# Kernel optimization log

Hardware: AMD Instinct MI355X
Metric: run time of the kernel (lower is better)

## Reference

```python
import jax, jax.numpy as jnp
import numpy as np

N_NODES = 100000
N_EDGES = 1600000
D = 128


def setup_inputs() -> dict:
    key = jax.random.key(0)
    k1, k2, k3, k4 = jax.random.split(key, 4)
    x = jax.random.normal(k1, (N_NODES, D), dtype=jnp.float32)
    # scale weights by 1/sqrt(fan_in) (matches typical init, keeps exp(e) stable)
    W = jax.random.normal(k2, (D, D), dtype=jnp.float32) / np.sqrt(D)
    a = jax.random.normal(k3, (2 * D,), dtype=jnp.float32) / np.sqrt(2 * D)
    edge_index = jax.random.randint(k4, (2, N_EDGES), 0, N_NODES, dtype=jnp.int64)
    return {"x": x, "W": W, "a": a, "edge_index": edge_index}


def reference(x, W, a, edge_index):
    # x: [N, in], W: [out, in] (torch Linear layout), a: [2*out], edge_index: [2, E]
    N = x.shape[0]
    d_out = W.shape[0]
    h = x @ W.T                                   # [N, out]
    src = edge_index[0]
    tgt = edge_index[1]
    # a(cat([h_src, h_tgt])) == h_src @ a[:d] + h_tgt @ a[d:] — avoids [E, 2d] concat
    s_src = h @ a[:d_out]                         # [N]
    s_tgt = h @ a[d_out:]                         # [N]
    e = jax.nn.leaky_relu(s_src[src] + s_tgt[tgt], negative_slope=0.2)  # [E]
    att = jnp.exp(e)                              # [E]
    att_sum = jax.ops.segment_sum(att, tgt, num_segments=N)             # [N]
    att_norm = att / (att_sum[tgt] + 1e-8)        # [E] (dropout=0 / eval mode)
    h_prime = jax.ops.segment_sum(h[src] * att_norm[:, None], tgt, num_segments=N)  # [N, out]
    h_prime = h_prime + x                          # residual (in_features == out_features)
    return jax.nn.elu(h_prime)
```

## Files before the change

kernel.cpp:

```cpp
#include <hip/hip_runtime.h>
#include <hip/hip_bf16.h>

#define DD 128
#define CAP 56
#define NBPW 128
#define CHUNK 4096
#define LBIN 832

typedef _Float16 half8  __attribute__((ext_vector_type(8)));
typedef _Float16 half2t __attribute__((ext_vector_type(2)));
typedef float f32x4 __attribute__((ext_vector_type(4)));

__device__ __forceinline__ ushort h16bits(float f) {
    _Float16 h = (_Float16)f;
    return __builtin_bit_cast(ushort, h);
}
__device__ __forceinline__ half8 pack8h(float4 lo, float4 hi) {
    half8 r;
    r[0] = (_Float16)lo.x; r[1] = (_Float16)lo.y;
    r[2] = (_Float16)lo.z; r[3] = (_Float16)lo.w;
    r[4] = (_Float16)hi.x; r[5] = (_Float16)hi.y;
    r[6] = (_Float16)hi.z; r[7] = (_Float16)hi.w;
    return r;
}
__device__ __forceinline__ float fdot2u(uint pair, uint avp, float c) {
    return __builtin_amdgcn_fdot2(__builtin_bit_cast(half2t, pair),
                                  __builtin_bit_cast(half2t, avp), c, false);
}

__global__ __launch_bounds__(256) void prep_w(
    const float* __restrict__ W, _Float16* __restrict__ Wh) {
    int i = blockIdx.x * 256 + threadIdx.x;
    if (i < DD * DD) Wh[i] = (_Float16)W[i];
}

__global__ __launch_bounds__(256, 2) void gemm_hist_kernel(
    const float* __restrict__ x, const _Float16* __restrict__ Wh,
    const float* __restrict__ a, ushort* __restrict__ h,
    float* __restrict__ ssrc, float* __restrict__ stgt,
    const int* __restrict__ tgt, int* __restrict__ H,
    int N, int E, int nbin, int nblk) {
    __shared__ ushort hl[4][16][136];
    __shared__ int lh[LBIN];
    const int wid = threadIdx.x >> 6;
    const int l   = threadIdx.x & 63;
    const int lr  = l & 15;
    const int lk  = l >> 4;

    half8 Bf[4][8];
    #pragma unroll
    for (int kt = 0; kt < 4; ++kt)
        #pragma unroll
        for (int n = 0; n < 8; ++n)
            Bf[kt][n] = *(const half8*)(Wh + (size_t)(n * 16 + lr) * DD + kt * 32 + lk * 8);
    float avs[8], avt[8];
    #pragma unroll
    for (int n = 0; n < 8; ++n) {
        avs[n] = a[n * 16 + lr];
        avt[n] = a[DD + n * 16 + lr];
    }

    const int rowBase = blockIdx.x * 64 + wid * 16;
    const int arow = rowBase + lr;
    f32x4 acc[8];
    #pragma unroll
    for (int n = 0; n < 8; ++n) acc[n] = (f32x4){0.f, 0.f, 0.f, 0.f};

    #pragma unroll
    for (int kt = 0; kt < 4; ++kt) {
        float4 x0, x1;
        if (arow < N) {
            const float* xp = x + (size_t)arow * DD + kt * 32 + lk * 8;
            x0 = *(const float4*)xp;
            x1 = *(const float4*)(xp + 4);
        } else {
            x0 = make_float4(0.f, 0.f, 0.f, 0.f);
            x1 = x0;
        }
        half8 A = pack8h(x0, x1);
        #pragma unroll
        for (int n = 0; n < 8; ++n)
            acc[n] = __builtin_amdgcn_mfma_f32_16x16x32_f16(A, Bf[kt][n], acc[n], 0, 0, 0);
    }

    float ps[4] = {0.f, 0.f, 0.f, 0.f}, pt[4] = {0.f, 0.f, 0.f, 0.f};
    #pragma unroll
    for (int n = 0; n < 8; ++n)
        #pragma unroll
        for (int r = 0; r < 4; ++r) {
            ps[r] = fmaf(acc[n][r], avs[n], ps[r]);
            pt[r] = fmaf(acc[n][r], avt[n], pt[r]);
        }
    #pragma unroll
    for (int r = 0; r < 4; ++r) {
        #pragma unroll
        for (int m = 8; m >= 1; m >>= 1) {
            ps[r] += __shfl_xor(ps[r], m);
            pt[r] += __shfl_xor(pt[r], m);
        }
    }
    if (lr == 0) {
        #pragma unroll
        for (int r = 0; r < 4; ++r) {
            int grow = rowBase + lk * 4 + r;
            if (grow < N) { ssrc[grow] = ps[r]; stgt[grow] = pt[r]; }
        }
    }

    #pragma unroll
    for (int n = 0; n < 8; ++n)
        #pragma unroll
        for (int r = 0; r < 4; ++r)
            hl[wid][lk * 4 + r][n * 16 + lr] = h16bits(acc[n][r]);
    __syncthreads();
    if (arow < N) {
        uint4* dst = (uint4*)(h + (size_t)arow * DD + lk * 32);
        const uint4* s4 = (const uint4*)&hl[wid][lr][lk * 32];
        dst[0] = s4[0]; dst[1] = s4[1]; dst[2] = s4[2]; dst[3] = s4[3];
    }

    if (blockIdx.x < nblk) {
        const int blk = blockIdx.x;
        for (int i = threadIdx.x; i < nbin; i += 256) lh[i] = 0;
        __syncthreads();
        const int base = blk * CHUNK;
        const int end = min(E, base + CHUNK);
        for (int e = base + threadIdx.x; e < end; e += 256)
            atomicAdd(&lh[tgt[e] >> 7], 1);
        __syncthreads();
        for (int i = threadIdx.x; i < nbin; i += 256) H[i * nblk + blk] = lh[i];
    }
}

__global__ __launch_bounds__(256) void p2a_colscan(
    int* __restrict__ H, int* __restrict__ binTot, int nblk) {
    __shared__ int lds[256];
    const int o = blockIdx.x * nblk;
    const int t = threadIdx.x;
    int a0 = (2 * t     < nblk) ? H[o + 2 * t]     : 0;
    int a1 = (2 * t + 1 < nblk) ? H[o + 2 * t + 1] : 0;
    int s = a0 + a1;
    lds[t] = s;
    __syncthreads();
    int val = s;
    for (int off = 1; off < 256; off <<= 1) {
        int u = (t >= off) ? lds[t - off] : 0;
        __syncthreads();
        val += u;
        lds[t] = val;
        __syncthreads();
    }
    int excl = val - s;
    if (2 * t     < nblk) H[o + 2 * t]     = excl;
    if (2 * t + 1 < nblk) H[o + 2 * t + 1] = excl + a0;
    if (t == 255) binTot[blockIdx.x] = val;
}

__device__ __forceinline__ void scan_bins(const int* __restrict__ binTot,
                                          int* __restrict__ binOffL, int nbin) {
    __shared__ int lds[256];
    const int t = threadIdx.x;
    int v[4];
    int s = 0;
    #pragma unroll
    for (int j = 0; j < 4; ++j) {
        int idx = t * 4 + j;
        v[j] = (idx < nbin) ? binTot[idx] : 0;
        s += v[j];
    }
    lds[t] = s;
    __syncthreads();
    int val = s;
    for (int off = 1; off < 256; off <<= 1) {
        int u = (t >= off) ? lds[t - off] : 0;
        __syncthreads();
        val += u;
        lds[t] = val;
        __syncthreads();
    }
    int excl = val - s;
    #pragma unroll
    for (int j = 0; j < 4; ++j) {
        int idx = t * 4 + j;
        if (idx < nbin) binOffL[idx] = excl;
        excl += v[j];
    }
    __syncthreads();
}

__global__ __launch_bounds__(256) void p3_partition(
    const int* __restrict__ src, const int* __restrict__ tgt,
    const int* __restrict__ H, const int* __restrict__ binTot,
    uint* __restrict__ ebuf, int E, int nbin, int nblk) {
    __shared__ int binOffL[LBIN];
    __shared__ int lcur[LBIN];
    scan_bins(binTot, binOffL, nbin);
    const int blk = blockIdx.x;
    for (int i = threadIdx.x; i < nbin; i += 256) lcur[i] = 0;
    __syncthreads();
    const int base = blk * CHUNK;
    const int end = min(E, base + CHUNK);
    for (int e = base + threadIdx.x; e < end; e += 256) {
        int s = src[e], t = tgt[e];
        int tb = t >> 7;
        int r = atomicAdd(&lcur[tb], 1);
        int slot = binOffL[tb] + H[tb * nblk + blk] + r;
        ebuf[slot] = ((uint)(t & 127) << 17) | (uint)s;
    }
}

__global__ __launch_bounds__(256) void p4_bucket(
    const uint* __restrict__ ebuf, const int* __restrict__ binTot,
    int* __restrict__ srcS, int* __restrict__ deg, int N, int nbin) {
    __shared__ int binOffL[LBIN];
    __shared__ int cur[NBPW];
    scan_bins(binTot, binOffL, nbin);
    const int bin = blockIdx.x;
    const int n0 = bin * NBPW;
    for (int i = threadIdx.x; i < NBPW; i += 256) cur[i] = 0;
    __syncthreads();
    const int beg = binOffL[bin];
    const int end = beg + binTot[bin];
    for (int i = beg + threadIdx.x; i < end; i += 256) {
        uint v = ebuf[i];
        int tl = (int)(v >> 17);
        int s  = (int)(v & 0x1FFFFu);
        int pos = atomicAdd(&cur[tl], 1);
        if (pos < CAP) srcS[(size_t)(n0 + tl) * CAP + pos] = s;
    }
    __syncthreads();
    for (int i = threadIdx.x; i < NBPW; i += 256) {
        int node = n0 + i;
        if (node < N) deg[node] = cur[i];
    }
}

__global__ __launch_bounds__(256) void gather_acc_kernel(
    const int* __restrict__ srcS, const int* __restrict__ degA,
    const float* __restrict__ ssrc, const float* __restrict__ stgt,
    const ushort* __restrict__ h, const float* __restrict__ x,
    float* __restrict__ out, int N) {
    __shared__ uint lds_pv[8][64];
    const int tid  = threadIdx.x;
    const int wid  = tid >> 6, lane = tid & 63;
    const int hw   = lane >> 5, hl = lane & 31;
    const int g    = hl >> 4,   l4 = hl & 15;
    const int nib  = (wid << 1) | hw;
    const int node = blockIdx.x * 8 + nib;
    if (node >= N) return;

    const float4 xv = *(const float4*)(x + (size_t)node * DD + l4 * 8 + g * 4);
    int deg = degA[node];
    if (deg > CAP) deg = CAP;
    const float st = stgt[node];
    const size_t base = (size_t)node * CAP;

    int sv0 = 0, sv1 = 0;
    float att0 = 0.f, att1 = 0.f;
    if (hl < deg) {
        sv0 = srcS[base + hl];
        float v = ssrc[sv0] + st;
        v = v > 0.f ? v : 0.2f * v;
        att0 = __expf(v);
    }
    if (hl + 32 < deg) {
        sv1 = srcS[base + hl + 32];
        float v = ssrc[sv1] + st;
        v = v > 0.f ? v : 0.2f * v;
        att1 = __expf(v);
    }
    float asum = att0 + att1;
    #pragma unroll
    for (int m = 16; m >= 1; m >>= 1) asum += __shfl_xor(asum, m);
    const float inv = 1.f / (asum + 1e-8f);
    lds_pv[nib][hl]      = ((uint)h16bits(att0) << 17) | (uint)sv0;
    lds_pv[nib][hl + 32] = ((uint)h16bits(att1) << 17) | (uint)sv1;

    const int passes = (deg + 1) >> 1;
    const uint* pvrow = lds_pv[nib];
    float acc[8] = {0.f, 0.f, 0.f, 0.f, 0.f, 0.f, 0.f, 0.f};

    #define PAIR_STEP(pv0, pv1)                                                  \
    {                                                                            \
        int s0 = (int)((pv0) & 0x1FFFFu), s1 = (int)((pv1) & 0x1FFFFu);          \
        uint4 hv0 = *(const uint4*)(h + ((size_t)s0 << 7) + (l4 << 3));          \
        uint4 hv1 = *(const uint4*)(h + ((size_t)s1 << 7) + (l4 << 3));          \
        uint avp = ((pv0) >> 17) | (((pv1) >> 17) << 16);                        \
        uint p0, p1;                                                             \
        p0 = __builtin_amdgcn_perm(hv1.x, hv0.x, 0x05040100u);                   \
        p1 = __builtin_amdgcn_perm(hv1.x, hv0.x, 0x07060302u);                   \
        acc[0] = fdot2u(p0, avp, acc[0]); acc[1] = fdot2u(p1, avp, acc[1]);      \
        p0 = __builtin_amdgcn_perm(hv1.y, hv0.y, 0x05040100u);                   \
        p1 = __builtin_amdgcn_perm(hv1.y, hv0.y, 0x07060302u);                   \
        acc[2] = fdot2u(p0, avp, acc[2]); acc[3] = fdot2u(p1, avp, acc[3]);      \
        p0 = __builtin_amdgcn_perm(hv1.z, hv0.z, 0x05040100u);                   \
        p1 = __builtin_amdgcn_perm(hv1.z, hv0.z, 0x07060302u);                   \
        acc[4] = fdot2u(p0, avp, acc[4]); acc[5] = fdot2u(p1, avp, acc[5]);      \
        p0 = __builtin_amdgcn_perm(hv1.w, hv0.w, 0x05040100u);                   \
        p1 = __builtin_amdgcn_perm(hv1.w, hv0.w, 0x07060302u);                   \
        acc[6] = fdot2u(p0, avp, acc[6]); acc[7] = fdot2u(p1, avp, acc[7]);      \
    }

    int p = 0;
    for (; p + 4 <= passes; p += 4) {
        const int i0 = (p << 1) + g;
        uint a0 = pvrow[i0], a1 = pvrow[i0 + 2];
        uint a2 = pvrow[i0 + 4], a3 = pvrow[i0 + 6];
        PAIR_STEP(a0, a1);
        PAIR_STEP(a2, a3);
    }
    if (p + 2 <= passes) {
        const int i0 = (p << 1) + g;
        uint a0 = pvrow[i0], a1 = pvrow[i0 + 2];
        PAIR_STEP(a0, a1);
        p += 2;
    }
    if (p < passes) {
        const int i0 = (p << 1) + g;
        uint a0 = pvrow[i0];
        int s0 = (int)(a0 & 0x1FFFFu);
        uint avp = a0 >> 17;
        uint4 hv0 = *(const uint4*)(h + ((size_t)s0 << 7) + (l4 << 3));
        acc[0] = fdot2u(hv0.x, avp, acc[0]); acc[1] = fdot2u(hv0.x >> 16, avp, acc[1]);
        acc[2] = fdot2u(hv0.y, avp, acc[2]); acc[3] = fdot2u(hv0.y >> 16, avp, acc[3]);
        acc[4] = fdot2u(hv0.z, avp, acc[4]); acc[5] = fdot2u(hv0.z >> 16, avp, acc[5]);
        acc[6] = fdot2u(hv0.w, avp, acc[6]); acc[7] = fdot2u(hv0.w >> 16, avp, acc[7]);
    }
    #undef PAIR_STEP

    #pragma unroll
    for (int j = 0; j < 8; ++j) acc[j] += __shfl_xor(acc[j], 16);

    float a0 = g ? acc[4] : acc[0];
    float a1 = g ? acc[5] : acc[1];
    float a2 = g ? acc[6] : acc[2];
    float a3 = g ? acc[7] : acc[3];
    float o0 = fmaf(a0, inv, xv.x), o1 = fmaf(a1, inv, xv.y);
    float o2 = fmaf(a2, inv, xv.z), o3 = fmaf(a3, inv, xv.w);
    o0 = o0 > 0.f ? o0 : expm1f(o0);
    o1 = o1 > 0.f ? o1 : expm1f(o1);
    o2 = o2 > 0.f ? o2 : expm1f(o2);
    o3 = o3 > 0.f ? o3 : expm1f(o3);
    *(float4*)(out + (size_t)node * DD + l4 * 8 + g * 4) = make_float4(o0, o1, o2, o3);
}

extern "C" void kernel_launch(void* const* d_in, const int* in_sizes, int n_in,
                              void* d_out, int out_size, void* d_ws, size_t ws_size,
                              hipStream_t stream) {
    const float* x  = (const float*)d_in[0];
    const float* W  = (const float*)d_in[1];
    const float* a  = (const float*)d_in[2];
    const int*   ei = (const int*)d_in[3];

    const int N = in_sizes[0] / DD;
    const int E = in_sizes[3] / 2;
    const int* src = ei;
    const int* tgt = ei + E;

    float* out = (float*)d_out;

    const int nbin = (N + NBPW - 1) / NBPW;
    const int nblk = (E + CHUNK - 1) / CHUNK;
    const int nTiles = (N + 63) / 64;

    char* w = (char*)d_ws;
    int*      srcS   = (int*)w;               w += (size_t)N * CAP * 4;
    ushort*   h      = (ushort*)w;            w += (size_t)N * DD * 2;
    float*    ssrc   = (float*)w;             w += (size_t)N * 4;
    float*    stgt   = (float*)w;             w += (size_t)N * 4;
    int*      deg    = (int*)w;               w += (size_t)N * 4;
    uint*     ebuf   = (uint*)w;              w += (size_t)E * 4;
    _Float16* Wh     = (_Float16*)w;          w += (size_t)DD * DD * 2;
    int*      H      = (int*)w;               w += (size_t)nbin * nblk * 4;
    int*      binTot = (int*)w;               w += (size_t)nbin * 4;

    prep_w<<<(DD * DD + 255) / 256, 256, 0, stream>>>(W, Wh);
    gemm_hist_kernel<<<nTiles, 256, 0, stream>>>(x, Wh, a, h, ssrc, stgt,
                                                 tgt, H, N, E, nbin, nblk);
    p2a_colscan<<<nbin, 256, 0, stream>>>(H, binTot, nblk);
    p3_partition<<<nblk, 256, 0, stream>>>(src, tgt, H, binTot, ebuf, E, nbin, nblk);
    p4_bucket<<<nbin, 256, 0, stream>>>(ebuf, binTot, srcS, deg, N, nbin);
    gather_acc_kernel<<<(N + 7) / 8, 256, 0, stream>>>(srcS, deg, ssrc, stgt,
                                                       h, x, out, N);
}
```

Baseline: 162.7 us.

## Shrink edge chunks, store histogram as ushort, cache per-block offsets in LDS

Cuts the edge chunk size from 4096 to 1024. This gives about four times more partition blocks, and spreads the histogram work across every GEMM block instead of only the first few hundred. To offset the larger block-by-bin histogram, the counts are stored as 16-bit values, and the column scan now processes eight entries per thread. The partition kernel loads its column of histogram offsets into shared memory once, instead of reading global memory on every edge. The risks are 16-bit overflow if a bin ever holds more than 65535 edges, and extra per-block overhead from the scan_bins prologue that each of the additional partition blocks repeats.

Result: slower. 174.7 us (+7.4%).

```diff
diff --git a/kernel.cpp b/kernel.cpp
--- a/kernel.cpp
+++ b/kernel.cpp
@@ -4,7 +4,7 @@
 #define DD 128
 #define CAP 56
 #define NBPW 128
-#define CHUNK 4096
+#define CHUNK 1024
 #define LBIN 832
 
 typedef _Float16 half8  __attribute__((ext_vector_type(8)));
@@ -38,7 +38,7 @@
     const float* __restrict__ x, const _Float16* __restrict__ Wh,
     const float* __restrict__ a, ushort* __restrict__ h,
     float* __restrict__ ssrc, float* __restrict__ stgt,
-    const int* __restrict__ tgt, int* __restrict__ H,
+    const int* __restrict__ tgt, ushort* __restrict__ H,
     int N, int E, int nbin, int nblk) {
     __shared__ ushort hl[4][16][136];
     __shared__ int lh[LBIN];
@@ -128,18 +128,24 @@
         for (int e = base + threadIdx.x; e < end; e += 256)
             atomicAdd(&lh[tgt[e] >> 7], 1);
         __syncthreads();
-        for (int i = threadIdx.x; i < nbin; i += 256) H[i * nblk + blk] = lh[i];
+        for (int i = threadIdx.x; i < nbin; i += 256)
+            H[(size_t)i * nblk + blk] = (ushort)lh[i];
     }
 }
 
 __global__ __launch_bounds__(256) void p2a_colscan(
-    int* __restrict__ H, int* __restrict__ binTot, int nblk) {
+    ushort* __restrict__ H, int* __restrict__ binTot, int nblk) {
     __shared__ int lds[256];
-    const int o = blockIdx.x * nblk;
+    const size_t o = (size_t)blockIdx.x * nblk;
     const int t = threadIdx.x;
-    int a0 = (2 * t     < nblk) ? H[o + 2 * t]     : 0;
-    int a1 = (2 * t + 1 < nblk) ? H[o + 2 * t + 1] : 0;
-    int s = a0 + a1;
+    int v[8];
+    int s = 0;
+    #pragma unroll
+    for (int j = 0; j < 8; ++j) {
+        int idx = t * 8 + j;
+        v[j] = (idx < nblk) ? (int)H[o + idx] : 0;
+        s += v[j];
+    }
     lds[t] = s;
     __syncthreads();
     int val = s;
@@ -151,8 +157,12 @@
         __syncthreads();
     }
     int excl = val - s;
-    if (2 * t     < nblk) H[o + 2 * t]     = excl;
-    if (2 * t + 1 < nblk) H[o + 2 * t + 1] = excl + a0;
+    #pragma unroll
+    for (int j = 0; j < 8; ++j) {
+        int idx = t * 8 + j;
+        if (idx < nblk) H[o + idx] = (ushort)excl;
+        excl += v[j];
+    }
     if (t == 255) binTot[blockIdx.x] = val;
 }
 
@@ -190,13 +200,17 @@
 
 __global__ __launch_bounds__(256) void p3_partition(
     const int* __restrict__ src, const int* __restrict__ tgt,
-    const int* __restrict__ H, const int* __restrict__ binTot,
+    const ushort* __restrict__ H, const int* __restrict__ binTot,
     uint* __restrict__ ebuf, int E, int nbin, int nblk) {
     __shared__ int binOffL[LBIN];
     __shared__ int lcur[LBIN];
+    __shared__ int HcolL[LBIN];
     scan_bins(binTot, binOffL, nbin);
     const int blk = blockIdx.x;
-    for (int i = threadIdx.x; i < nbin; i += 256) lcur[i] = 0;
+    for (int i = threadIdx.x; i < nbin; i += 256) {
+        lcur[i] = 0;
+        HcolL[i] = (int)H[(size_t)i * nblk + blk];
+    }
     __syncthreads();
     const int base = blk * CHUNK;
     const int end = min(E, base + CHUNK);
@@ -204,7 +218,7 @@
         int s = src[e], t = tgt[e];
         int tb = t >> 7;
         int r = atomicAdd(&lcur[tb], 1);
-        int slot = binOffL[tb] + H[tb * nblk + blk] + r;
+        int slot = binOffL[tb] + HcolL[tb] + r;
         ebuf[slot] = ((uint)(t & 127) << 17) | (uint)s;
     }
 }
@@ -371,7 +385,7 @@
     int*      deg    = (int*)w;               w += (size_t)N * 4;
     uint*     ebuf   = (uint*)w;              w += (size_t)E * 4;
     _Float16* Wh     = (_Float16*)w;          w += (size_t)DD * DD * 2;
-    int*      H      = (int*)w;               w += (size_t)nbin * nblk * 4;
+    ushort*   H      = (ushort*)w;            w += (size_t)nbin * nblk * 2;
     int*      binTot = (int*)w;               w += (size_t)nbin * 4;
 
     prep_w<<<(DD * DD + 255) / 256, 256, 0, stream>>>(W, Wh);
```

## Fuse bucketing into gather via LDS buckets, shrink bins, compact histogram

Applied to the files above, without the earlier changes.

The per-bin bucket pass and the per-node gather kernel are merged into one kernel. It builds each 64-node bin's source lists in shared memory and then computes attention and aggregation for those nodes directly. This removes the global srcS/deg round trip and one launch. The histogram is stored as ushort in a blk-major layout, and the bin prefix scan moves into a single dedicated kernel instead of being redone in every block. The fused kernel launches far fewer blocks, each processing 8 nodes per wave serially, which risks lower parallelism and latency hiding in the gather.

Measured after the change: 160.6 us. About the same (-1.3%).

```diff
diff --git a/kernel.cpp b/kernel.cpp
--- a/kernel.cpp
+++ b/kernel.cpp
@@ -3,9 +3,9 @@
 
 #define DD 128
 #define CAP 56
-#define NBPW 128
+#define NBPW 64
 #define CHUNK 4096
-#define LBIN 832
+#define LBIN 1600
 
 typedef _Float16 half8  __attribute__((ext_vector_type(8)));
 typedef _Float16 half2t __attribute__((ext_vector_type(2)));
@@ -38,7 +38,7 @@
     const float* __restrict__ x, const _Float16* __restrict__ Wh,
     const float* __restrict__ a, ushort* __restrict__ h,
     float* __restrict__ ssrc, float* __restrict__ stgt,
-    const int* __restrict__ tgt, int* __restrict__ H,
+    const int* __restrict__ tgt, ushort* __restrict__ H,
     int N, int E, int nbin, int nblk) {
     __shared__ ushort hl[4][16][136];
     __shared__ int lh[LBIN];
@@ -126,19 +126,20 @@
         const int base = blk * CHUNK;
         const int end = min(E, base + CHUNK);
         for (int e = base + threadIdx.x; e < end; e += 256)
-            atomicAdd(&lh[tgt[e] >> 7], 1);
-        __syncthreads();
-        for (int i = threadIdx.x; i < nbin; i += 256) H[i * nblk + blk] = lh[i];
+            atomicAdd(&lh[tgt[e] >> 6], 1);
+        __syncthreads();
+        ushort* Hrow = H + (size_t)blk * nbin;
+        for (int i = threadIdx.x; i < nbin; i += 256) Hrow[i] = (ushort)lh[i];
     }
 }
 
 __global__ __launch_bounds__(256) void p2a_colscan(
-    int* __restrict__ H, int* __restrict__ binTot, int nblk) {
+    ushort* __restrict__ H, int* __restrict__ binTot, int nbin, int nblk) {
     __shared__ int lds[256];
-    const int o = blockIdx.x * nblk;
+    const int bin = blockIdx.x;
     const int t = threadIdx.x;
-    int a0 = (2 * t     < nblk) ? H[o + 2 * t]     : 0;
-    int a1 = (2 * t + 1 < nblk) ? H[o + 2 * t + 1] : 0;
+    int a0 = (2 * t     < nblk) ? (int)H[(size_t)(2 * t)     * nbin + bin] : 0;
+    int a1 = (2 * t + 1 < nblk) ? (int)H[(size_t)(2 * t + 1) * nbin + bin] : 0;
     int s = a0 + a1;
     lds[t] = s;
     __syncthreads();
@@ -151,20 +152,20 @@
         __syncthreads();
     }
     int excl = val - s;
-    if (2 * t     < nblk) H[o + 2 * t]     = excl;
-    if (2 * t + 1 < nblk) H[o + 2 * t + 1] = excl + a0;
+    if (2 * t     < nblk) H[(size_t)(2 * t)     * nbin + bin] = (ushort)excl;
+    if (2 * t + 1 < nblk) H[(size_t)(2 * t + 1) * nbin + bin] = (ushort)(excl + a0);
     if (t == 255) binTot[blockIdx.x] = val;
 }
 
-__device__ __forceinline__ void scan_bins(const int* __restrict__ binTot,
-                                          int* __restrict__ binOffL, int nbin) {
+__global__ __launch_bounds__(256) void p2b_binscan(
+    const int* __restrict__ binTot, int* __restrict__ binOff, int nbin) {
     __shared__ int lds[256];
     const int t = threadIdx.x;
-    int v[4];
+    int v[8];
     int s = 0;
     #pragma unroll
-    for (int j = 0; j < 4; ++j) {
-        int idx = t * 4 + j;
+    for (int j = 0; j < 8; ++j) {
+        int idx = t * 8 + j;
         v[j] = (idx < nbin) ? binTot[idx] : 0;
         s += v[j];
     }
@@ -180,168 +181,164 @@
     }
     int excl = val - s;
     #pragma unroll
-    for (int j = 0; j < 4; ++j) {
-        int idx = t * 4 + j;
-        if (idx < nbin) binOffL[idx] = excl;
+    for (int j = 0; j < 8; ++j) {
+        int idx = t * 8 + j;
+        if (idx < nbin) binOff[idx] = excl;
         excl += v[j];
     }
-    __syncthreads();
+    if (t == 255) binOff[nbin] = val;
 }
 
 __global__ __launch_bounds__(256) void p3_partition(
     const int* __restrict__ src, const int* __restrict__ tgt,
-    const int* __restrict__ H, const int* __restrict__ binTot,
+    const ushort* __restrict__ H, const int* __restrict__ binOff,
     uint* __restrict__ ebuf, int E, int nbin, int nblk) {
-    __shared__ int binOffL[LBIN];
+    __shared__ int slotBase[LBIN];
     __shared__ int lcur[LBIN];
-    scan_bins(binTot, binOffL, nbin);
     const int blk = blockIdx.x;
-    for (int i = threadIdx.x; i < nbin; i += 256) lcur[i] = 0;
+    const ushort* Hrow = H + (size_t)blk * nbin;
+    for (int i = threadIdx.x; i < nbin; i += 256) {
+        slotBase[i] = binOff[i] + (int)Hrow[i];
+        lcur[i] = 0;
+    }
     __syncthreads();
     const int base = blk * CHUNK;
     const int end = min(E, base + CHUNK);
     for (int e = base + threadIdx.x; e < end; e += 256) {
         int s = src[e], t = tgt[e];
-        int tb = t >> 7;
+        int tb = t >> 6;
         int r = atomicAdd(&lcur[tb], 1);
-        int slot = binOffL[tb] + H[tb * nblk + blk] + r;
-        ebuf[slot] = ((uint)(t & 127) << 17) | (uint)s;
-    }
-}
-
-__global__ __launch_bounds__(256) void p4_bucket(
-    const uint* __restrict__ ebuf, const int* __restrict__ binTot,
-    int* __restrict__ srcS, int* __restrict__ deg, int N, int nbin) {
-    __shared__ int binOffL[LBIN];
-    __shared__ int cur[NBPW];
-    scan_bins(binTot, binOffL, nbin);
-    const int bin = blockIdx.x;
-    const int n0 = bin * NBPW;
-    for (int i = threadIdx.x; i < NBPW; i += 256) cur[i] = 0;
-    __syncthreads();
-    const int beg = binOffL[bin];
-    const int end = beg + binTot[bin];
-    for (int i = beg + threadIdx.x; i < end; i += 256) {
-        uint v = ebuf[i];
-        int tl = (int)(v >> 17);
-        int s  = (int)(v & 0x1FFFFu);
-        int pos = atomicAdd(&cur[tl], 1);
-        if (pos < CAP) srcS[(size_t)(n0 + tl) * CAP + pos] = s;
-    }
-    __syncthreads();
-    for (int i = threadIdx.x; i < NBPW; i += 256) {
-        int node = n0 + i;
-        if (node < N) deg[node] = cur[i];
-    }
-}
-
-__global__ __launch_bounds__(256) void gather_acc_kernel(
-    const int* __restrict__ srcS, const int* __restrict__ degA,
+        int slot = slotBase[tb] + r;
+        ebuf[slot] = ((uint)(t & 63) << 17) | (uint)s;
+    }
+}
+
+__global__ __launch_bounds__(256) void bucket_gather_kernel(
+    const uint* __restrict__ ebuf, const int* __restrict__ binOff,
     const float* __restrict__ ssrc, const float* __restrict__ stgt,
     const ushort* __restrict__ h, const float* __restrict__ x,
     float* __restrict__ out, int N) {
+    __shared__ uint bucket[NBPW][CAP];
+    __shared__ int  cur[NBPW];
     __shared__ uint lds_pv[8][64];
-    const int tid  = threadIdx.x;
-    const int wid  = tid >> 6, lane = tid & 63;
-    const int hw   = lane >> 5, hl = lane & 31;
-    const int g    = hl >> 4,   l4 = hl & 15;
-    const int nib  = (wid << 1) | hw;
-    const int node = blockIdx.x * 8 + nib;
-    if (node >= N) return;
-
-    const float4 xv = *(const float4*)(x + (size_t)node * DD + l4 * 8 + g * 4);
-    int deg = degA[node];
-    if (deg > CAP) deg = CAP;
-    const float st = stgt[node];
-    const size_t base = (size_t)node * CAP;
-
-    int sv0 = 0, sv1 = 0;
-    float att0 = 0.f, att1 = 0.f;
-    if (hl < deg) {
-        sv0 = srcS[base + hl];
-        float v = ssrc[sv0] + st;
-        v = v > 0.f ? v : 0.2f * v;
-        att0 = __expf(v);
-    }
-    if (hl + 32 < deg) {
-        sv1 = srcS[base + hl + 32];
-        float v = ssrc[sv1] + st;
-        v = v > 0.f ? v : 0.2f * v;
-        att1 = __expf(v);
-    }
-    float asum = att0 + att1;
-    #pragma unroll
-    for (int m = 16; m >= 1; m >>= 1) asum += __shfl_xor(asum, m);
-    const float inv = 1.f / (asum + 1e-8f);
-    lds_pv[nib][hl]      = ((uint)h16bits(att0) << 17) | (uint)sv0;
-    lds_pv[nib][hl + 32] = ((uint)h16bits(att1) << 17) | (uint)sv1;
-
-    const int passes = (deg + 1) >> 1;
-    const uint* pvrow = lds_pv[nib];
-    float acc[8] = {0.f, 0.f, 0.f, 0.f, 0.f, 0.f, 0.f, 0.f};
-
-    #define PAIR_STEP(pv0, pv1)                                                  \
-    {                                                                            \
-        int s0 = (int)((pv0) & 0x1FFFFu), s1 = (int)((pv1) & 0x1FFFFu);          \
-        uint4 hv0 = *(const uint4*)(h + ((size_t)s0 << 7) + (l4 << 3));          \
-        uint4 hv1 = *(const uint4*)(h + ((size_t)s1 << 7) + (l4 << 3));          \
-        uint avp = ((pv0) >> 17) | (((pv1) >> 17) << 16);                        \
-        uint p0, p1;                                                             \
-        p0 = __builtin_amdgcn_perm(hv1.x, hv0.x, 0x05040100u);                   \
-        p1 = __builtin_amdgcn_perm(hv1.x, hv0.x, 0x07060302u);                   \
-        acc[0] = fdot2u(p0, avp, acc[0]); acc[1] = fdot2u(p1, avp, acc[1]);      \
-        p0 = __builtin_amdgcn_perm(hv1.y, hv0.y, 0x05040100u);                   \
-        p1 = __builtin_amdgcn_perm(hv1.y, hv0.y, 0x07060302u);                   \
-        acc[2] = fdot2u(p0, avp, acc[2]); acc[3] = fdot2u(p1, avp, acc[3]);      \
-        p0 = __builtin_amdgcn_perm(hv1.z, hv0.z, 0x05040100u);                   \
-        p1 = __builtin_amdgcn_perm(hv1.z, hv0.z, 0x07060302u);                   \
-        acc[4] = fdot2u(p0, avp, acc[4]); acc[5] = fdot2u(p1, avp, acc[5]);      \
-        p0 = __builtin_amdgcn_perm(hv1.w, hv0.w, 0x05040100u);                   \
-        p1 = __builtin_amdgcn_perm(hv1.w, hv0.w, 0x07060302u);                   \
-        acc[6] = fdot2u(p0, avp, acc[6]); acc[7] = fdot2u(p1, avp, acc[7]);      \
-    }
-
-    int p = 0;
-    for (; p + 4 <= passes; p += 4) {
-        const int i0 = (p << 1) + g;
-        uint a0 = pvrow[i0], a1 = pvrow[i0 + 2];
-        uint a2 = pvrow[i0 + 4], a3 = pvrow[i0 + 6];
-        PAIR_STEP(a0, a1);
-        PAIR_STEP(a2, a3);
-    }
-    if (p + 2 <= passes) {
-        const int i0 = (p << 1) + g;
-        uint a0 = pvrow[i0], a1 = pvrow[i0 + 2];
-        PAIR_STEP(a0, a1);
-        p += 2;
-    }
-    if (p < passes) {
-        const int i0 = (p << 1) + g;
-        uint a0 = pvrow[i0];
-        int s0 = (int)(a0 & 0x1FFFFu);
-        uint avp = a0 >> 17;
-        uint4 hv0 = *(const uint4*)(h + ((size_t)s0 << 7) + (l4 << 3));
-        acc[0] = fdot2u(hv0.x, avp, acc[0]); acc[1] = fdot2u(hv0.x >> 16, avp, acc[1]);
-        acc[2] = fdot2u(hv0.y, avp, acc[2]); acc[3] = fdot2u(hv0.y >> 16, avp, acc[3]);
-        acc[4] = fdot2u(hv0.z, avp, acc[4]); acc[5] = fdot2u(hv0.z >> 16, avp, acc[5]);
-        acc[6] = fdot2u(hv0.w, avp, acc[6]); acc[7] = fdot2u(hv0.w >> 16, avp, acc[7]);
-    }
-    #undef PAIR_STEP
-
-    #pragma unroll
-    for (int j = 0; j < 8; ++j) acc[j] += __shfl_xor(acc[j], 16);
-
-    float a0 = g ? acc[4] : acc[0];
-    float a1 = g ? acc[5] : acc[1];
-    float a2 = g ? acc[6] : acc[2];
-    float a3 = g ? acc[7] : acc[3];
-    float o0 = fmaf(a0, inv, xv.x), o1 = fmaf(a1, inv, xv.y);
-    float o2 = fmaf(a2, inv, xv.z), o3 = fmaf(a3, inv, xv.w);
-    o0 = o0 > 0.f ? o0 : expm1f(o0);
-    o1 = o1 > 0.f ? o1 : expm1f(o1);
-    o2 = o2 > 0.f ? o2 : expm1f(o2);
-    o3 = o3 > 0.f ? o3 : expm1f(o3);
-    *(float4*)(out + (size_t)node * DD + l4 * 8 + g * 4) = make_float4(o0, o1, o2, o3);
+    const int bin = blockIdx.x;
+    const int n0 = bin << 6;
+    const int tid = threadIdx.x;
+
+    for (int i = tid; i < NBPW; i += 256) cur[i] = 0;
+    __syncthreads();
+    const int beg = binOff[bin], end = binOff[bin + 1];
+    for (int i = beg + tid; i < end; i += 256) {
+        uint v = ebuf[i];
+        int tl = (int)(v >> 17);
+        int pos = atomicAdd(&cur[tl], 1);
+        if (pos < CAP) bucket[tl][pos] = v & 0x1FFFFu;
+    }
+    __syncthreads();
+
+    const int wid = tid >> 6, lane = tid & 63;
+    const int hw = lane >> 5, hl = lane & 31;
+    const int g  = hl >> 4,   l4 = hl & 15;
+    const int nib = (wid << 1) | hw;
+
+    for (int it = 0; it < 8; ++it) {
+        const int nloc = (wid << 4) + (it << 1) + hw;
+        const int node = n0 + nloc;
+        if (node >= N) continue;
+
+        const float4 xv = *(const float4*)(x + (size_t)node * DD + l4 * 8 + g * 4);
+        int deg = cur[nloc];
+        if (deg > CAP) deg = CAP;
+        const float st = stgt[node];
+
+        int sv0 = 0, sv1 = 0;
+        float att0 = 0.f, att1 = 0.f;
+        if (hl < deg) {
+            sv0 = (int)bucket[nloc][hl];
+            float v = ssrc[sv0] + st;
+            v = v > 0.f ? v : 0.2f * v;
+            att0 = __expf(v);
+        }
+        if (hl + 32 < deg) {
+            sv1 = (int)bucket[nloc][hl + 32];
+            float v = ssrc[sv1] + st;
+            v = v > 0.f ? v : 0.2f * v;
+            att1 = __expf(v);
+        }
+        float asum = att0 + att1;
+        #pragma unroll
+        for (int m = 16; m >= 1; m >>= 1) asum += __shfl_xor(asum, m);
+        const float inv = 1.f / (asum + 1e-8f);
+        lds_pv[nib][hl]      = ((uint)h16bits(att0) << 17) | (uint)sv0;
+        lds_pv[nib][hl + 32] = ((uint)h16bits(att1) << 17) | (uint)sv1;
+
+        const int passes = (deg + 1) >> 1;
+        const uint* pvrow = lds_pv[nib];
+        float acc[8] = {0.f, 0.f, 0.f, 0.f, 0.f, 0.f, 0.f, 0.f};
+
+        #define PAIR_STEP(pv0, pv1)                                              \
+        {                                                                        \
+            int s0 = (int)((pv0) & 0x1FFFFu), s1 = (int)((pv1) & 0x1FFFFu);      \
+            uint4 hv0 = *(const uint4*)(h + ((size_t)s0 << 7) + (l4 << 3));      \
+            uint4 hv1 = *(const uint4*)(h + ((size_t)s1 << 7) + (l4 << 3));      \
+            uint avp = ((pv0) >> 17) | (((pv1) >> 17) << 16);                    \
+            uint p0, p1;                                                         \
+            p0 = __builtin_amdgcn_perm(hv1.x, hv0.x, 0x05040100u);               \
+            p1 = __builtin_amdgcn_perm(hv1.x, hv0.x, 0x07060302u);               \
+            acc[0] = fdot2u(p0, avp, acc[0]); acc[1] = fdot2u(p1, avp, acc[1]);  \
+            p0 = __builtin_amdgcn_perm(hv1.y, hv0.y, 0x05040100u);               \
+            p1 = __builtin_amdgcn_perm(hv1.y, hv0.y, 0x07060302u);               \
+            acc[2] = fdot2u(p0, avp, acc[2]); acc[3] = fdot2u(p1, avp, acc[3]);  \
+            p0 = __builtin_amdgcn_perm(hv1.z, hv0.z, 0x05040100u);               \
+            p1 = __builtin_amdgcn_perm(hv1.z, hv0.z, 0x07060302u);               \
+            acc[4] = fdot2u(p0, avp, acc[4]); acc[5] = fdot2u(p1, avp, acc[5]);  \
+            p0 = __builtin_amdgcn_perm(hv1.w, hv0.w, 0x05040100u);               \
+            p1 = __builtin_amdgcn_perm(hv1.w, hv0.w, 0x07060302u);               \
+            acc[6] = fdot2u(p0, avp, acc[6]); acc[7] = fdot2u(p1, avp, acc[7]);  \
+        }
+
+        int p = 0;
+        for (; p + 4 <= passes; p += 4) {
+            const int i0 = (p << 1) + g;
+            uint a0 = pvrow[i0], a1 = pvrow[i0 + 2];
+            uint a2 = pvrow[i0 + 4], a3 = pvrow[i0 + 6];
+            PAIR_STEP(a0, a1);
+            PAIR_STEP(a2, a3);
+        }
+        if (p + 2 <= passes) {
+            const int i0 = (p << 1) + g;
+            uint a0 = pvrow[i0], a1 = pvrow[i0 + 2];
+            PAIR_STEP(a0, a1);
+            p += 2;
+        }
+        if (p < passes) {
+            const int i0 = (p << 1) + g;
+            uint a0 = pvrow[i0];
+            int s0 = (int)(a0 & 0x1FFFFu);
+            uint avp = a0 >> 17;
+            uint4 hv0 = *(const uint4*)(h + ((size_t)s0 << 7) + (l4 << 3));
+            acc[0] = fdot2u(hv0.x, avp, acc[0]); acc[1] = fdot2u(hv0.x >> 16, avp, acc[1]);
+            acc[2] = fdot2u(hv0.y, avp, acc[2]); acc[3] = fdot2u(hv0.y >> 16, avp, acc[3]);
+            acc[4] = fdot2u(hv0.z, avp, acc[4]); acc[5] = fdot2u(hv0.z >> 16, avp, acc[5]);
+            acc[6] = fdot2u(hv0.w, avp, acc[6]); acc[7] = fdot2u(hv0.w >> 16, avp, acc[7]);
+        }
+        #undef PAIR_STEP
+
+        #pragma unroll
+        for (int j = 0; j < 8; ++j) acc[j] += __shfl_xor(acc[j], 16);
+
+        float a0 = g ? acc[4] : acc[0];
+        float a1 = g ? acc[5] : acc[1];
+        float a2 = g ? acc[6] : acc[2];
+        float a3 = g ? acc[7] : acc[3];
+        float o0 = fmaf(a0, inv, xv.x), o1 = fmaf(a1, inv, xv.y);
+        float o2 = fmaf(a2, inv, xv.z), o3 = fmaf(a3, inv, xv.w);
+        o0 = o0 > 0.f ? o0 : expm1f(o0);
+        o1 = o1 > 0.f ? o1 : expm1f(o1);
+        o2 = o2 > 0.f ? o2 : expm1f(o2);
+        o3 = o3 > 0.f ? o3 : expm1f(o3);
+        *(float4*)(out + (size_t)node * DD + l4 * 8 + g * 4) = make_float4(o0, o1, o2, o3);
+    }
 }
 
 extern "C" void kernel_launch(void* const* d_in, const int* in_sizes, int n_in,
@@ -363,23 +360,24 @@
     const int nblk = (E + CHUNK - 1) / CHUNK;
     const int nTiles = (N + 63) / 64;
 
+    #define ALIGN256(v) (((size_t)(v) + 255) & ~(size_t)255)
     char* w = (char*)d_ws;
-    int*      srcS   = (int*)w;               w += (size_t)N * CAP * 4;
-    ushort*   h      = (ushort*)w;            w += (size_t)N * DD * 2;
-    float*    ssrc   = (float*)w;             w += (size_t)N * 4;
-    float*    stgt   = (float*)w;             w += (size_t)N * 4;
-    int*      deg    = (int*)w;               w += (size_t)N * 4;
-    uint*     ebuf   = (uint*)w;              w += (size_t)E * 4;
-    _Float16* Wh     = (_Float16*)w;          w += (size_t)DD * DD * 2;
-    int*      H      = (int*)w;               w += (size_t)nbin * nblk * 4;
-    int*      binTot = (int*)w;               w += (size_t)nbin * 4;
+    ushort*   h      = (ushort*)w;            w += ALIGN256((size_t)N * DD * 2);
+    float*    ssrc   = (float*)w;             w += ALIGN256((size_t)N * 4);
+    float*    stgt   = (float*)w;             w += ALIGN256((size_t)N * 4);
+    uint*     ebuf   = (uint*)w;              w += ALIGN256((size_t)E * 4);
+    _Float16* Wh     = (_Float16*)w;          w += ALIGN256((size_t)DD * DD * 2);
+    ushort*   H      = (ushort*)w;            w += ALIGN256((size_t)nblk * nbin * 2);
+    int*      binTot = (int*)w;               w += ALIGN256((size_t)nbin * 4);
+    int*      binOff = (int*)w;               w += ALIGN256((size_t)(nbin + 1) * 4);
+    #undef ALIGN256
 
     prep_w<<<(DD * DD + 255) / 256, 256, 0, stream>>>(W, Wh);
     gemm_hist_kernel<<<nTiles, 256, 0, stream>>>(x, Wh, a, h, ssrc, stgt,
                                                  tgt, H, N, E, nbin, nblk);
-    p2a_colscan<<<nbin, 256, 0, stream>>>(H, binTot, nblk);
-    p3_partition<<<nblk, 256, 0, stream>>>(src, tgt, H, binTot, ebuf, E, nbin, nblk);
-    p4_bucket<<<nbin, 256, 0, stream>>>(ebuf, binTot, srcS, deg, N, nbin);
-    gather_acc_kernel<<<(N + 7) / 8, 256, 0, stream>>>(srcS, deg, ssrc, stgt,
-                                                       h, x, out, N);
-}
+    p2a_colscan<<<nbin, 256, 0, stream>>>(H, binTot, nbin, nblk);
+    p2b_binscan<<<1, 256, 0, stream>>>(binTot, binOff, nbin);
+    p3_partition<<<nblk, 256, 0, stream>>>(src, tgt, H, binOff, ebuf, E, nbin, nblk);
+    bucket_gather_kernel<<<nbin, 256, 0, stream>>>(ebuf, binOff, ssrc, stgt,
+                                                   h, x, out, N);
+}
```
